# Kernel optimization log

Hardware: AMD Instinct MI355X
Metric: run time of the kernel (lower is better)

The kernel has to match this reference:

```python
import jax, jax.numpy as jnp
import numpy as np

# ---- static configuration (mirrors C4WithSyscalls __init__/_build_keys) ----
MEM = 16384            # memory_size
OUT = 64               # output_size
NCTX = MEM + 5 + OUT   # context: [memory, PC, SP, BP, AX, OUT_LEN, output]
SCALE = 10.0
GATE_SCALE = 20.0
ADDR_BITS = int(np.ceil(np.log2(NCTX)))   # 15
TYPE_BITS = 5
KDIM = ADDR_BITS + TYPE_BITS
POWERS = jnp.asarray(2 ** np.arange(ADDR_BITS), jnp.int32)

# opcode values for the 15 experts: IMM,LEA,ADD,SUB,MUL,DIV,MOD,SHL,SHR,EQ,NE,LT,GT,LE,GE
OP_VALS = jnp.asarray([1., 2., 9., 10., 11., 12., 13., 14., 15., 3., 4., 5., 6., 7., 8.], jnp.float32)
# binary ops (everything except IMM, LEA) pop the stack: sp += 8
POP_MASK = jnp.asarray([0., 0.] + [1.] * 13, jnp.float32)


def _build_keys():
    addrs = np.arange(NCTX)
    bits = (addrs[:, None] // (2 ** np.arange(ADDR_BITS))) % 2
    addr_keys = (2.0 * bits - 1.0) * SCALE                       # [N, ADDR_BITS]
    type_tags = np.full((NCTX, TYPE_BITS), -SCALE)
    type_tags[MEM, 0] = SCALE      # PC
    type_tags[MEM + 1, 1] = SCALE  # SP
    type_tags[MEM + 2, 2] = SCALE  # BP
    type_tags[MEM + 3, 3] = SCALE  # AX
    type_tags[MEM + 4:, 4] = SCALE  # OUT_LEN + output slots
    return jnp.asarray(np.concatenate([addr_keys, type_tags], 1), jnp.float32)

KEYS = _build_keys()  # [NCTX, KDIM]


def silu_threshold(x, scale=GATE_SCALE):
    d = scale * x
    return (jax.nn.silu(d + 0.5 * scale) - jax.nn.silu(d - 0.5 * scale)) / scale


def eq_gate(a, b, scale=GATE_SCALE):
    diff = a - b
    return silu_threshold(diff + 0.5, scale) * silu_threshold(-diff + 0.5, scale)


def attend(context, addr):
    """Soft-addressed gather: context [B,NCTX], addr [B] float -> (value [B], weights [B,NCTX])."""
    ai = jnp.clip(addr, 0.0, float(NCTX - 1)).astype(jnp.int32)
    bits = (ai[:, None] // POWERS) % 2
    addr_q = (2.0 * bits.astype(jnp.float32) - 1.0) * SCALE                 # [B, ADDR_BITS]
    type_q = jnp.full((addr.shape[0], TYPE_BITS), -SCALE, jnp.float32)      # memory_type tag
    q = jnp.concatenate([addr_q, type_q], axis=1)                           # [B, KDIM]
    scores = jnp.einsum('nd,bd->bn', KEYS, q) / np.sqrt(KDIM)
    w = jax.nn.softmax(scores, axis=1)
    return jnp.einsum('bn,bn->b', w, context), w


def expert_outputs(a, b, imm, bp):
    """a = stack_top, b = ax. Returns [B, 15] new-ax candidates per expert."""
    safeb = jnp.where(jnp.abs(b) < 1e-6, 1e-6, b)
    div = a / safeb
    mod = a - safeb * jnp.floor(div)
    sh = jnp.clip(b, 0.0, 31.0)
    eq = eq_gate(a, b)
    lt = jax.nn.sigmoid(GATE_SCALE * (b - a - 0.5))
    gt = jax.nn.sigmoid(GATE_SCALE * (a - b - 0.5))
    return jnp.stack([
        imm,               # IMM
        bp + imm,          # LEA
        a + b,             # ADD
        a - b,             # SUB
        a * b,             # MUL
        div,               # DIV
        mod,               # MOD
        a * jnp.exp2(sh),  # SHL
        a * jnp.exp2(-sh), # SHR
        eq,                # EQ
        1.0 - eq,          # NE
        lt,                # LT
        gt,                # GT
        1.0 - gt,          # LE
        1.0 - lt,          # GE
    ], axis=-1)


def _forward(memory, output, ax, pc, sp, bp, out_len, num_steps):
    B = memory.shape[0]
    pcf, spf, bpf = pc.astype(jnp.float32), sp.astype(jnp.float32), bp.astype(jnp.float32)
    olf = out_len.astype(jnp.float32)[:, None]

    def step(carry, _):
        pc_, sp_, bp_, ax_, mem_ = carry
        regs = jnp.stack([pc_, sp_, bp_, ax_], axis=1)                    # [B,4]
        context = jnp.concatenate([mem_, regs, olf, output], axis=1)     # [B,NCTX]
        inst, _ = attend(context, pc_)
        imm = jnp.floor(inst / 256.0)
        opcode = inst - imm * 256.0
        stack_top, w_sp = attend(context, sp_)
        gates = eq_gate(opcode[:, None], OP_VALS[None, :])                # [B,15] soft top-1
        outs = expert_outputs(stack_top, ax_, imm, bp_)                   # [B,15]
        gsum = gates.sum(-1)
        new_ax = (gates * outs).sum(-1) + (1.0 - gsum) * ax_              # NoOp default
        pop_g = (gates * POP_MASK).sum(-1)
        new_sp = sp_ + 8.0 * pop_g
        new_pc = pc_ + 8.0
        # soft scatter: write new_ax back at the (soft) stack-top address
        new_mem = mem_ + pop_g[:, None] * w_sp[:, :MEM] * (new_ax[:, None] - mem_)
        return (new_pc, new_sp, bp_, new_ax, new_mem), None

    carry, _ = jax.lax.scan(step, (pcf, spf, bpf, ax, memory), None, length=num_steps)
    return carry[4]  # final memory [B, MEM]


def setup_inputs() -> dict:
    key = jax.random.key(0)
    k = jax.random.split(key, 8)
    B = 1024
    return {
        'memory': jax.random.normal(k[0], (B, MEM), jnp.float32),
        'output': jax.random.normal(k[1], (B, OUT), jnp.float32),
        'ax': jax.random.normal(k[2], (B,), jnp.float32),
        'pc': jax.random.randint(k[3], (B,), 0, MEM, jnp.int32),
        'sp': jax.random.randint(k[4], (B,), 0, MEM, jnp.int32),
        'bp': jax.random.randint(k[5], (B,), 0, MEM, jnp.int32),
        'out_len': jax.random.randint(k[6], (B,), 0, OUT, jnp.int32),
        'num_steps': 16,
    }


def reference(memory, output, ax, pc, sp, bp, out_len, num_steps):
    return _forward(memory, output, ax, pc, sp, bp, out_len, num_steps)
```

## Files before the change

kernel.cpp:

```cpp
#include <hip/hip_runtime.h>
#include <math.h>

#define MEMSZ 16384
#define NCTX  16453

typedef float f4 __attribute__((ext_vector_type(4)));

__device__ __forceinline__ float sigmoidf_(float x) {
    return __builtin_amdgcn_rcpf(1.0f + __expf(-x));
}
__device__ __forceinline__ float siluf_(float x) {
    return x * sigmoidf_(x);
}
__device__ __forceinline__ float silu_thr(float x) {
    float d = 20.0f * x;
    return (siluf_(d + 10.0f) - siluf_(d - 10.0f)) * 0.05f;
}
__device__ __forceinline__ float eq_gate_d(float diff) {
    return silu_thr(diff + 0.5f) * silu_thr(0.5f - diff);
}

__global__ __launch_bounds__(256) void copy_kernel(const f4* __restrict__ src,
                                                   f4* __restrict__ dst, int n4) {
    int i = blockIdx.x * blockDim.x + threadIdx.x;
    if (i < n4)
        __builtin_nontemporal_store(__builtin_nontemporal_load(&src[i]), &dst[i]);
}

__global__ __launch_bounds__(64) void sim_kernel(
        float* __restrict__ mem,
        const float* __restrict__ outp,
        const float* __restrict__ ax_in,
        const int* __restrict__ pc_in,
        const int* __restrict__ sp_in,
        const int* __restrict__ bp_in,
        const int* __restrict__ ol_in,
        const int* __restrict__ nstep,
        int B) {
    int b = blockIdx.x * 64 + threadIdx.x;
    if (b >= B) return;

    float* __restrict__ mrow = mem + (size_t)b * MEMSZ;
    const float* __restrict__ orow = outp + (size_t)b * 64;

    float pc0 = (float)pc_in[b];
    float sp  = (float)sp_in[b];
    float bp  = (float)bp_in[b];
    float ax  = ax_in[b];
    float olf = (float)ol_in[b];
    int   T   = nstep[0];

    const float opv[15] = {1.f, 2.f, 9.f, 10.f, 11.f, 12.f, 13.f, 14.f, 15.f,
                           3.f, 4.f, 5.f, 6.f, 7.f, 8.f};

    if (T == 16) {
        float pf[16];
        int   pfi[16];
#pragma unroll
        for (int t = 0; t < 16; ++t) {
            float pcr = pc0 + 8.0f * (float)t;
            float a1 = fminf(fmaxf(pcr, 0.0f), (float)(NCTX - 1));
            int ai = (int)a1;
            pfi[t] = ai;
            int pidx = (ai < MEMSZ) ? ai : ai - MEMSZ;
            pf[t] = mrow[pidx];
        }

        int   sidx[16];
        float sval[16];
#pragma unroll
        for (int j = 0; j < 16; ++j) { sidx[j] = -1; sval[j] = 0.0f; }

        float a2 = fminf(fmaxf(sp, 0.0f), (float)(NCTX - 1));
        int   si  = (int)a2;
        int   tgt = (si < MEMSZ) ? si : si - MEMSZ;
        float raw = mrow[tgt];

#pragma unroll
        for (int t = 0; t < 16; ++t) {
            float pcr = pc0 + 8.0f * (float)t;

            int ai   = pfi[t];
            int pidx = (ai < MEMSZ) ? ai : ai - MEMSZ;
            float m_pc = pf[t];
#pragma unroll
            for (int j = 0; j < 16; ++j)
                if (j < t && sidx[j] == pidx) m_pc = sval[j];

            float inst;
            if (ai < MEMSZ) {
                inst = m_pc;
            } else {
                int r = ai - MEMSZ;
                float cv = (r == 0) ? pcr
                         : (r == 1) ? sp
                         : (r == 2) ? bp
                         : (r == 3) ? ax
                         : (r == 4) ? olf
                                    : orow[r - 5];
                inst = 0.5f * (cv + m_pc);
            }
            float imm = floorf(inst * (1.0f / 256.0f));
            float opc = inst - imm * 256.0f;

            float g[15];
#pragma unroll
            for (int j = 0; j < 15; ++j) g[j] = eq_gate_d(opc - opv[j]);
            float gsum = 0.0f;
#pragma unroll
            for (int j = 0; j < 15; ++j) gsum += g[j];
            float pop = 0.0f;
#pragma unroll
            for (int j = 2; j < 15; ++j) pop += g[j];

            float sp_next = sp + 8.0f * pop;
            int   si_n = 0, tgt_n = 0;
            float raw_n = 0.0f;
            if (t < 15) {
                float a2n = fminf(fmaxf(sp_next, 0.0f), (float)(NCTX - 1));
                si_n  = (int)a2n;
                tgt_n = (si_n < MEMSZ) ? si_n : si_n - MEMSZ;
                raw_n = mrow[tgt_n];
            }

            float mtv = raw;
#pragma unroll
            for (int j = 0; j < 16; ++j)
                if (j < t && sidx[j] == tgt) mtv = sval[j];

            float stv, wfac;
            if (si < MEMSZ) {
                stv = mtv;
                wfac = 1.0f;
            } else {
                int r = si - MEMSZ;
                float cv = (r == 0) ? pcr
                         : (r == 1) ? sp
                         : (r == 2) ? bp
                         : (r == 3) ? ax
                         : (r == 4) ? olf
                                    : orow[r - 5];
                stv = 0.5f * (cv + mtv);
                wfac = 0.5f;
            }

            float a = stv, bv = ax;
            float safeb = (fabsf(bv) < 1e-6f) ? 1e-6f : bv;
            float dvv = a / safeb;
            float md  = a - safeb * floorf(dvv);
            float sh  = fminf(fmaxf(bv, 0.0f), 31.0f);
            float eqg = eq_gate_d(a - bv);
            float lt  = sigmoidf_(20.0f * (bv - a - 0.5f));
            float gt  = sigmoidf_(20.0f * (a - bv - 0.5f));
            float outs[15] = {
                imm, bp + imm, a + bv, a - bv, a * bv, dvv, md,
                a * exp2f(sh), a * exp2f(-sh),
                eqg, 1.0f - eqg, lt, gt, 1.0f - gt, 1.0f - lt
            };
            float acc = 0.0f;
#pragma unroll
            for (int j = 0; j < 15; ++j) acc += g[j] * outs[j];
            float nax = acc + (1.0f - gsum) * ax;

            float vnew = mtv + pop * wfac * (nax - mtv);
            mrow[tgt] = vnew;
            sidx[t] = tgt;
            sval[t] = vnew;

            sp = sp_next;
            ax = nax;
            if (t < 15) { si = si_n; tgt = tgt_n; raw = raw_n; }
        }
    } else {
        float pc = pc0;
        for (int t = 0; t < T; ++t) {
            float a1 = fminf(fmaxf(pc, 0.0f), (float)(NCTX - 1));
            int   ai = (int)a1;
            float a2 = fminf(fmaxf(sp, 0.0f), (float)(NCTX - 1));
            int   si = (int)a2;
            int pidx   = (ai < MEMSZ) ? ai : (ai - MEMSZ);
            int target = (si < MEMSZ) ? si : (si - MEMSZ);
            float m_pc = mrow[pidx];
            float mtv  = mrow[target];

            float inst;
            if (ai < MEMSZ) {
                inst = m_pc;
            } else {
                int r = ai - MEMSZ;
                float cv = (r == 0) ? pc
                         : (r == 1) ? sp
                         : (r == 2) ? bp
                         : (r == 3) ? ax
                         : (r == 4) ? olf
                                    : orow[r - 5];
                inst = 0.5f * (cv + m_pc);
            }
            float imm = floorf(inst * (1.0f / 256.0f));
            float opc = inst - imm * 256.0f;

            float stv, wfac;
            if (si < MEMSZ) {
                stv = mtv;
                wfac = 1.0f;
            } else {
                int r = si - MEMSZ;
                float cv = (r == 0) ? pc
                         : (r == 1) ? sp
                         : (r == 2) ? bp
                         : (r == 3) ? ax
                         : (r == 4) ? olf
                                    : orow[r - 5];
                stv = 0.5f * (cv + mtv);
                wfac = 0.5f;
            }

            float a = stv, bv = ax;
            float safeb = (fabsf(bv) < 1e-6f) ? 1e-6f : bv;
            float dvv = a / safeb;
            float md  = a - safeb * floorf(dvv);
            float sh  = fminf(fmaxf(bv, 0.0f), 31.0f);
            float eqg = eq_gate_d(a - bv);
            float lt  = sigmoidf_(20.0f * (bv - a - 0.5f));
            float gt  = sigmoidf_(20.0f * (a - bv - 0.5f));
            float outs[15] = {
                imm, bp + imm, a + bv, a - bv, a * bv, dvv, md,
                a * exp2f(sh), a * exp2f(-sh),
                eqg, 1.0f - eqg, lt, gt, 1.0f - gt, 1.0f - lt
            };

            float gsum = 0.0f, acc = 0.0f, pop = 0.0f;
#pragma unroll
            for (int j = 0; j < 15; ++j) {
                float gg = eq_gate_d(opc - opv[j]);
                gsum += gg;
                acc  += gg * outs[j];
                if (j >= 2) pop += gg;
            }
            float nax = acc + (1.0f - gsum) * ax;

            mrow[target] = mtv + pop * wfac * (nax - mtv);

            sp = sp + 8.0f * pop;
            pc = pc + 8.0f;
            ax = nax;
        }
    }
}

extern "C" void kernel_launch(void* const* d_in, const int* in_sizes, int n_in,
                              void* d_out, int out_size, void* d_ws, size_t ws_size,
                              hipStream_t stream) {
    const float* memory = (const float*)d_in[0];
    const float* output = (const float*)d_in[1];
    const float* ax     = (const float*)d_in[2];
    const int*   pc     = (const int*)d_in[3];
    const int*   sp     = (const int*)d_in[4];
    const int*   bp     = (const int*)d_in[5];
    const int*   ol     = (const int*)d_in[6];
    const int*   ns     = (const int*)d_in[7];

    int B = in_sizes[0] / MEMSZ;
    int n4 = (B * MEMSZ) / 4;

    hipLaunchKernelGGL(copy_kernel, dim3((n4 + 255) / 256), dim3(256), 0, stream,
                       (const f4*)memory, (f4*)d_out, n4);
    hipLaunchKernelGGL(sim_kernel, dim3((B + 63) / 64), dim3(64), 0, stream,
                       (float*)d_out, output, ax, pc, sp, bp, ol, ns, B);
}
```

Measured before the change: 156.4 us.

## Assign one wavefront per batch row and spread gate evaluation across lanes

The simulation kernel now launches one 64-lane block per batch row instead of one thread per row. In the T==16 path each lane computes one of the 15 opcode gates, and the results are gathered with shuffles. Only lane 0 writes memory, and the generic path runs on lane 0 alone. This spreads the serial dependency chain over many more wavefronts and GPU units, at the cost of redundant per-lane work (the loads and arithmetic are repeated on every lane) and many shuffles per step.

```diff
diff --git a/kernel.cpp b/kernel.cpp
--- a/kernel.cpp
+++ b/kernel.cpp
@@ -37,8 +37,9 @@
         const int* __restrict__ ol_in,
         const int* __restrict__ nstep,
         int B) {
-    int b = blockIdx.x * 64 + threadIdx.x;
+    int b = blockIdx.x;
     if (b >= B) return;
+    int lane = threadIdx.x;
 
     float* __restrict__ mrow = mem + (size_t)b * MEMSZ;
     const float* __restrict__ orow = outp + (size_t)b * 64;
@@ -50,8 +51,10 @@
     float olf = (float)ol_in[b];
     int   T   = nstep[0];
 
-    const float opv[15] = {1.f, 2.f, 9.f, 10.f, 11.f, 12.f, 13.f, 14.f, 15.f,
-                           3.f, 4.f, 5.f, 6.f, 7.f, 8.f};
+    float opvl = (lane < 2)  ? (float)(lane + 1)
+               : (lane < 9)  ? (float)(lane + 7)
+               : (lane < 15) ? (float)(lane - 6)
+                             : 0.0f;
 
     if (T == 16) {
         float pf[16];
@@ -103,15 +106,22 @@
             float imm = floorf(inst * (1.0f / 256.0f));
             float opc = inst - imm * 256.0f;
 
-            float g[15];
-#pragma unroll
-            for (int j = 0; j < 15; ++j) g[j] = eq_gate_d(opc - opv[j]);
+            float gl = eq_gate_d(opc - opvl);
+
+            float G0  = __shfl(gl, 0),  G1  = __shfl(gl, 1),  G2  = __shfl(gl, 2);
+            float G3  = __shfl(gl, 3),  G4  = __shfl(gl, 4),  G5  = __shfl(gl, 5);
+            float G6  = __shfl(gl, 6),  G7  = __shfl(gl, 7),  G8  = __shfl(gl, 8);
+            float G9  = __shfl(gl, 9),  G10 = __shfl(gl, 10), G11 = __shfl(gl, 11);
+            float G12 = __shfl(gl, 12), G13 = __shfl(gl, 13), G14 = __shfl(gl, 14);
+
             float gsum = 0.0f;
-#pragma unroll
-            for (int j = 0; j < 15; ++j) gsum += g[j];
+            gsum += G0;  gsum += G1;  gsum += G2;  gsum += G3;  gsum += G4;
+            gsum += G5;  gsum += G6;  gsum += G7;  gsum += G8;  gsum += G9;
+            gsum += G10; gsum += G11; gsum += G12; gsum += G13; gsum += G14;
             float pop = 0.0f;
-#pragma unroll
-            for (int j = 2; j < 15; ++j) pop += g[j];
+            pop += G2;  pop += G3;  pop += G4;  pop += G5;  pop += G6;
+            pop += G7;  pop += G8;  pop += G9;  pop += G10; pop += G11;
+            pop += G12; pop += G13; pop += G14;
 
             float sp_next = sp + 8.0f * pop;
             int   si_n = 0, tgt_n = 0;
@@ -135,6 +145,83 @@
             } else {
                 int r = si - MEMSZ;
                 float cv = (r == 0) ? pcr
+                         : (r == 1) ? sp
+                         : (r == 2) ? bp
+                         : (r == 3) ? ax
+                         : (r == 4) ? olf
+                                    : orow[r - 5];
+                stv = 0.5f * (cv + mtv);
+                wfac = 0.5f;
+            }
+
+            float a = stv, bv = ax;
+            float safeb = (fabsf(bv) < 1e-6f) ? 1e-6f : bv;
+            float dvv = a / safeb;
+            float md  = a - safeb * floorf(dvv);
+            float sh  = fminf(fmaxf(bv, 0.0f), 31.0f);
+            float eqg = eq_gate_d(a - bv);
+            float lt  = sigmoidf_(20.0f * (bv - a - 0.5f));
+            float gt  = sigmoidf_(20.0f * (a - bv - 0.5f));
+            float o0 = imm,            o1 = bp + imm,     o2 = a + bv;
+            float o3 = a - bv,         o4 = a * bv,       o5 = dvv;
+            float o6 = md,             o7 = a * exp2f(sh), o8 = a * exp2f(-sh);
+            float o9 = eqg,            o10 = 1.0f - eqg,  o11 = lt;
+            float o12 = gt,            o13 = 1.0f - gt,   o14 = 1.0f - lt;
+
+            float acc = 0.0f;
+            acc += G0 * o0;   acc += G1 * o1;   acc += G2 * o2;
+            acc += G3 * o3;   acc += G4 * o4;   acc += G5 * o5;
+            acc += G6 * o6;   acc += G7 * o7;   acc += G8 * o8;
+            acc += G9 * o9;   acc += G10 * o10; acc += G11 * o11;
+            acc += G12 * o12; acc += G13 * o13; acc += G14 * o14;
+            float nax = acc + (1.0f - gsum) * ax;
+
+            float vnew = mtv + pop * wfac * (nax - mtv);
+            if (lane == 0) mrow[tgt] = vnew;
+            sidx[t] = tgt;
+            sval[t] = vnew;
+
+            sp = sp_next;
+            ax = nax;
+            if (t < 15) { si = si_n; tgt = tgt_n; raw = raw_n; }
+        }
+    } else if (lane == 0) {
+        const float opv[15] = {1.f, 2.f, 9.f, 10.f, 11.f, 12.f, 13.f, 14.f, 15.f,
+                               3.f, 4.f, 5.f, 6.f, 7.f, 8.f};
+        float pc = pc0;
+        for (int t = 0; t < T; ++t) {
+            float a1 = fminf(fmaxf(pc, 0.0f), (float)(NCTX - 1));
+            int   ai = (int)a1;
+            float a2 = fminf(fmaxf(sp, 0.0f), (float)(NCTX - 1));
+            int   si = (int)a2;
+            int pidx   = (ai < MEMSZ) ? ai : (ai - MEMSZ);
+            int target = (si < MEMSZ) ? si : (si - MEMSZ);
+            float m_pc = mrow[pidx];
+            float mtv  = mrow[target];
+
+            float inst;
+            if (ai < MEMSZ) {
+                inst = m_pc;
+            } else {
+                int r = ai - MEMSZ;
+                float cv = (r == 0) ? pc
+                         : (r == 1) ? sp
+                         : (r == 2) ? bp
+                         : (r == 3) ? ax
+                         : (r == 4) ? olf
+                                    : orow[r - 5];
+                inst = 0.5f * (cv + m_pc);
+            }
+            float imm = floorf(inst * (1.0f / 256.0f));
+            float opc = inst - imm * 256.0f;
+
+            float stv, wfac;
+            if (si < MEMSZ) {
+                stv = mtv;
+                wfac = 1.0f;
+            } else {
+                int r = si - MEMSZ;
+                float cv = (r == 0) ? pc
                          : (r == 1) ? sp
                          : (r == 2) ? bp
                          : (r == 3) ? ax
@@ -157,77 +244,6 @@
                 a * exp2f(sh), a * exp2f(-sh),
                 eqg, 1.0f - eqg, lt, gt, 1.0f - gt, 1.0f - lt
             };
-            float acc = 0.0f;
-#pragma unroll
-            for (int j = 0; j < 15; ++j) acc += g[j] * outs[j];
-            float nax = acc + (1.0f - gsum) * ax;
-
-            float vnew = mtv + pop * wfac * (nax - mtv);
-            mrow[tgt] = vnew;
-            sidx[t] = tgt;
-            sval[t] = vnew;
-
-            sp = sp_next;
-            ax = nax;
-            if (t < 15) { si = si_n; tgt = tgt_n; raw = raw_n; }
-        }
-    } else {
-        float pc = pc0;
-        for (int t = 0; t < T; ++t) {
-            float a1 = fminf(fmaxf(pc, 0.0f), (float)(NCTX - 1));
-            int   ai = (int)a1;
-            float a2 = fminf(fmaxf(sp, 0.0f), (float)(NCTX - 1));
-            int   si = (int)a2;
-            int pidx   = (ai < MEMSZ) ? ai : (ai - MEMSZ);
-            int target = (si < MEMSZ) ? si : (si - MEMSZ);
-            float m_pc = mrow[pidx];
-            float mtv  = mrow[target];
-
-            float inst;
-            if (ai < MEMSZ) {
-                inst = m_pc;
-            } else {
-                int r = ai - MEMSZ;
-                float cv = (r == 0) ? pc
-                         : (r == 1) ? sp
-                         : (r == 2) ? bp
-                         : (r == 3) ? ax
-                         : (r == 4) ? olf
-                                    : orow[r - 5];
-                inst = 0.5f * (cv + m_pc);
-            }
-            float imm = floorf(inst * (1.0f / 256.0f));
-            float opc = inst - imm * 256.0f;
-
-            float stv, wfac;
-            if (si < MEMSZ) {
-                stv = mtv;
-                wfac = 1.0f;
-            } else {
-                int r = si - MEMSZ;
-                float cv = (r == 0) ? pc
-                         : (r == 1) ? sp
-                         : (r == 2) ? bp
-                         : (r == 3) ? ax
-                         : (r == 4) ? olf
-                                    : orow[r - 5];
-                stv = 0.5f * (cv + mtv);
-                wfac = 0.5f;
-            }
-
-            float a = stv, bv = ax;
-            float safeb = (fabsf(bv) < 1e-6f) ? 1e-6f : bv;
-            float dvv = a / safeb;
-            float md  = a - safeb * floorf(dvv);
-            float sh  = fminf(fmaxf(bv, 0.0f), 31.0f);
-            float eqg = eq_gate_d(a - bv);
-            float lt  = sigmoidf_(20.0f * (bv - a - 0.5f));
-            float gt  = sigmoidf_(20.0f * (a - bv - 0.5f));
-            float outs[15] = {
-                imm, bp + imm, a + bv, a - bv, a * bv, dvv, md,
-                a * exp2f(sh), a * exp2f(-sh),
-                eqg, 1.0f - eqg, lt, gt, 1.0f - gt, 1.0f - lt
-            };
 
             float gsum = 0.0f, acc = 0.0f, pop = 0.0f;
 #pragma unroll
@@ -265,6 +281,6 @@
 
     hipLaunchKernelGGL(copy_kernel, dim3((n4 + 255) / 256), dim3(256), 0, stream,
                        (const f4*)memory, (f4*)d_out, n4);
-    hipLaunchKernelGGL(sim_kernel, dim3((B + 63) / 64), dim3(64), 0, stream,
+    hipLaunchKernelGGL(sim_kernel, dim3(B), dim3(64), 0, stream,
                        (float*)d_out, output, ax, pc, sp, bp, ol, ns, B);
 }
```

Result: faster. 147.0 us (-6.0%).
